# Optimization experiments

Measured on AMD Instinct MI355X. Metric: run time of the kernel, lower is better.

## Reference

```python
import jax, jax.numpy as jnp
import numpy as np

EPS = 1e-5

def _bn(h, gamma, beta):
    # BatchNorm1d in training mode: biased batch stats over the batch dim
    m = h.mean(axis=0)
    v = h.var(axis=0)
    return gamma * (h - m) * jax.lax.rsqrt(v + EPS) + beta


def setup_inputs() -> dict:
    key = jax.random.key(0)
    ks = jax.random.split(key, 8)
    N, E, D = 100000, 1000000, 64
    x = jax.random.normal(ks[0], (N, D), dtype=jnp.float32)
    pair_features = jax.random.normal(ks[1], (E, D), dtype=jnp.float32)
    pair_index = jax.random.randint(ks[2], (2, E), 0, N, dtype=jnp.int32)
    s = 1.0 / np.sqrt(D)
    W_atom = jax.random.uniform(ks[3], (D, D), jnp.float32, -s, s)
    b_atom = jnp.zeros((D,), jnp.float32)
    g_atom = jnp.ones((D,), jnp.float32)
    be_atom = jnp.zeros((D,), jnp.float32)
    W_pair = jax.random.uniform(ks[4], (D, D), jnp.float32, -s, s)
    b_pair = jnp.zeros((D,), jnp.float32)
    g_pair = jnp.ones((D,), jnp.float32)
    be_pair = jnp.zeros((D,), jnp.float32)
    s2 = 1.0 / np.sqrt(2 * D)
    W_a2p = jax.random.uniform(ks[5], (2 * D, D), jnp.float32, -s2, s2)
    b_a2p = jnp.zeros((D,), jnp.float32)
    return {
        "x": x, "pair_features": pair_features, "pair_index": pair_index,
        "W_atom": W_atom, "b_atom": b_atom, "g_atom": g_atom, "be_atom": be_atom,
        "W_pair": W_pair, "b_pair": b_pair, "g_pair": g_pair, "be_pair": be_pair,
        "W_a2p": W_a2p, "b_a2p": b_a2p,
    }


def reference(x, pair_features, pair_index,
              W_atom, b_atom, g_atom, be_atom,
              W_pair, b_pair, g_pair, be_pair,
              W_a2p, b_a2p):
    # atom path: Linear -> ReLU -> BatchNorm
    atom_out = _bn(jax.nn.relu(x @ W_atom + b_atom), g_atom, be_atom)
    # pair path: gather send/recv atoms, concat, linear
    send = x[pair_index[0]]                       # [E, D]
    recv = x[pair_index[1]]                       # [E, D]
    pair_input = jnp.concatenate([send, recv], axis=-1)  # [E, 2D]
    a2p = pair_input @ W_a2p + b_a2p              # [E, Dp]
    pair_bn = _bn(jax.nn.relu(pair_features @ W_pair + b_pair), g_pair, be_pair)
    return atom_out, a2p + pair_bn
```

## Files before the change

kernel.cpp:

```cpp
#include <hip/hip_runtime.h>

#define D 64
#define EPS 1e-5f

typedef __bf16 bf16x8 __attribute__((ext_vector_type(8)));
typedef float  f32x4  __attribute__((ext_vector_type(4)));

#define MFMA(a, b, c) __builtin_amdgcn_mfma_f32_16x16x32_bf16((a), (b), (c), 0, 0, 0)

static inline int imin(int a, int b) { return a < b ? a : b; }

template <bool NTLOAD>
__global__ void __launch_bounds__(256) fused_h_stats_kernel(
    const float* __restrict__ in, const float* __restrict__ W,
    const float* __restrict__ bias, int nrows,
    float* __restrict__ stats, __bf16* __restrict__ hout)
{
    const int tid = threadIdx.x;
    const int lane = tid & 63, wv = tid >> 6;
    const int q = lane >> 4, l16 = lane & 15;

    bf16x8 Bf[2][4];
#pragma unroll
    for (int ks = 0; ks < 2; ++ks)
#pragma unroll
      for (int nt = 0; nt < 4; ++nt)
#pragma unroll
        for (int j = 0; j < 8; ++j)
          Bf[ks][nt][j] = (__bf16)W[(ks * 32 + q * 8 + j) * 64 + nt * 16 + l16];

    float bc[4];
#pragma unroll
    for (int nt = 0; nt < 4; ++nt) bc[nt] = bias[nt * 16 + l16];

    float s[4] = {0.f, 0.f, 0.f, 0.f}, sq[4] = {0.f, 0.f, 0.f, 0.f};
    const f32x4 ZERO = {0.f, 0.f, 0.f, 0.f};

    const int ntiles = (nrows + 31) >> 5;
    const int stride = gridDim.x << 2;
    for (int t = (blockIdx.x << 2) + wv; t < ntiles; t += stride) {
        f32x4 st[2][2][2];
#pragma unroll
        for (int mt = 0; mt < 2; ++mt) {
            int arow = (t << 5) + mt * 16 + l16;
            arow = arow < nrows ? arow : nrows - 1;
            const float* p = in + (size_t)arow * 64 + q * 8;
#pragma unroll
            for (int ks = 0; ks < 2; ++ks) {
                if (NTLOAD) {
                    st[mt][ks][0] = __builtin_nontemporal_load((const f32x4*)(p + ks * 32));
                    st[mt][ks][1] = __builtin_nontemporal_load((const f32x4*)(p + ks * 32 + 4));
                } else {
                    st[mt][ks][0] = *(const f32x4*)(p + ks * 32);
                    st[mt][ks][1] = *(const f32x4*)(p + ks * 32 + 4);
                }
            }
        }

        bf16x8 af[2][2];
#pragma unroll
        for (int mt = 0; mt < 2; ++mt)
#pragma unroll
          for (int ks = 0; ks < 2; ++ks)
#pragma unroll
            for (int j = 0; j < 8; ++j)
              af[mt][ks][j] = (__bf16)st[mt][ks][j >> 2][j & 3];

        f32x4 acc[2][4];
#pragma unroll
        for (int mt = 0; mt < 2; ++mt)
#pragma unroll
          for (int nt = 0; nt < 4; ++nt) {
            acc[mt][nt] = MFMA(af[mt][0], Bf[0][nt], ZERO);
            acc[mt][nt] = MFMA(af[mt][1], Bf[1][nt], acc[mt][nt]);
          }

#pragma unroll
        for (int mt = 0; mt < 2; ++mt) {
            bf16x8 hh[2];
#pragma unroll
            for (int nt = 0; nt < 4; ++nt)
#pragma unroll
              for (int r = 0; r < 4; ++r) {
                const int row = (t << 5) + mt * 16 + q * 4 + r;
                float h = fmaxf(acc[mt][nt][r] + bc[nt], 0.f);
                if (row < nrows) { s[nt] += h; sq[nt] = fmaf(h, h, sq[nt]); }
                hh[nt >> 1][(nt & 1) * 4 + r] = (__bf16)h;
              }
            if (((2 * t + mt) << 4) < nrows) {
                __bf16* dst = hout + ((size_t)(2 * t + mt) * 2048 + lane * 16);
                *(bf16x8*)dst = hh[0];
                *(bf16x8*)(dst + 8) = hh[1];
            }
        }
    }

#pragma unroll
    for (int nt = 0; nt < 4; ++nt) {
        s[nt]  += __shfl_xor(s[nt], 16, 64);  s[nt]  += __shfl_xor(s[nt], 32, 64);
        sq[nt] += __shfl_xor(sq[nt], 16, 64); sq[nt] += __shfl_xor(sq[nt], 32, 64);
    }
    if (q == 0) {
#pragma unroll
        for (int nt = 0; nt < 4; ++nt) {
            atomicAdd(&stats[nt * 16 + l16], s[nt]);
            atomicAdd(&stats[64 + nt * 16 + l16], sq[nt]);
        }
    }
}

__global__ void finalize_stats_kernel(
    const float* __restrict__ stats,
    const float* __restrict__ g_a, const float* __restrict__ be_a,
    const float* __restrict__ g_p, const float* __restrict__ be_p,
    float n_atom, float n_pair, float* __restrict__ params)
{
    const int t = threadIdx.x;
    const int j = t & 63;
    const bool p = t >= 64;
    const float* st = stats + (p ? 128 : 0);
    const float* g  = p ? g_p  : g_a;
    const float* be = p ? be_p : be_a;
    const float cnt = p ? n_pair : n_atom;
    float m = st[j] / cnt;
    float v = st[64 + j] / cnt - m * m;
    float sc = g[j] * rsqrtf(v + EPS);
    float sh = be[j] - m * sc;
    float* pr = params + (p ? 128 : 0);
    pr[j] = sc;
    pr[64 + j] = sh;
}

__global__ void __launch_bounds__(256) apply_atom_kernel(
    float* __restrict__ out, const float* __restrict__ params, int nrows)
{
    const int tid = threadIdx.x;
    const int lane = tid & 63, wv = tid >> 6;
    const int q = lane >> 4, l16 = lane & 15;

    float sc[4], sh[4];
#pragma unroll
    for (int nt = 0; nt < 4; ++nt) {
        sc[nt] = params[nt * 16 + l16];
        sh[nt] = params[64 + nt * 16 + l16];
    }

    const int ntiles = (nrows + 15) >> 4;
    const int stride = gridDim.x << 2;
    for (int t = (blockIdx.x << 2) + wv; t < ntiles; t += stride) {
        const __bf16* src = (const __bf16*)out + ((size_t)t * 2048 + lane * 16);
        bf16x8 h0 = *(const bf16x8*)src;
        bf16x8 h1 = *(const bf16x8*)(src + 8);
        asm volatile("s_waitcnt vmcnt(0)" ::: "memory");
#pragma unroll
        for (int nt = 0; nt < 4; ++nt)
#pragma unroll
          for (int r = 0; r < 4; ++r) {
            const int row = (t << 4) + q * 4 + r;
            float h = (float)((nt < 2) ? h0[nt * 4 + r] : h1[(nt - 2) * 4 + r]);
            if (row < nrows)
                __builtin_nontemporal_store(fmaf(h, sc[nt], sh[nt]),
                                            out + (size_t)row * 64 + nt * 16 + l16);
          }
    }
}

__global__ void __launch_bounds__(256) pair_pass2_kernel(
    float* __restrict__ out, const float* __restrict__ x,
    const int* __restrict__ pidx,
    const float* __restrict__ Wa, const float* __restrict__ ba,
    int E, const float* __restrict__ params)
{
    const int tid = threadIdx.x;
    const int lane = tid & 63, wv = tid >> 6;
    const int q = lane >> 4, l16 = lane & 15;

    bf16x8 B2[4][4];
#pragma unroll
    for (int ks = 0; ks < 4; ++ks)
#pragma unroll
      for (int nt = 0; nt < 4; ++nt)
#pragma unroll
        for (int j = 0; j < 8; ++j)
          B2[ks][nt][j] = (__bf16)Wa[(ks * 32 + q * 8 + j) * 64 + nt * 16 + l16];

    float bac[4], sc[4], sh[4];
#pragma unroll
    for (int nt = 0; nt < 4; ++nt) {
        bac[nt] = ba[nt * 16 + l16];
        sc[nt]  = params[nt * 16 + l16];
        sh[nt]  = params[64 + nt * 16 + l16];
    }

    const f32x4 ZERO = {0.f, 0.f, 0.f, 0.f};

    const int ntiles = E >> 4;
    const int stride = gridDim.x << 2;
    for (int t = (blockIdx.x << 2) + wv; t < ntiles; t += stride) {
        const int e0 = t << 4;
        const int se = pidx[e0 + l16];
        const int re = pidx[E + e0 + l16];
        const float* ps = x + (size_t)se * 64 + q * 8;
        const float* pr = x + (size_t)re * 64 + q * 8;

        f32x4 g[4][2];
        g[0][0] = *(const f32x4*)ps;          g[0][1] = *(const f32x4*)(ps + 4);
        g[1][0] = *(const f32x4*)(ps + 32);   g[1][1] = *(const f32x4*)(ps + 36);
        g[2][0] = *(const f32x4*)pr;          g[2][1] = *(const f32x4*)(pr + 4);
        g[3][0] = *(const f32x4*)(pr + 32);   g[3][1] = *(const f32x4*)(pr + 36);

        const __bf16* hsrc = (const __bf16*)out + ((size_t)t * 2048 + lane * 16);
        bf16x8 h0 = *(const bf16x8*)hsrc;
        bf16x8 h1 = *(const bf16x8*)(hsrc + 8);

        bf16x8 af[4];
#pragma unroll
        for (int ks = 0; ks < 4; ++ks)
#pragma unroll
          for (int j = 0; j < 8; ++j)
            af[ks][j] = (__bf16)g[ks][j >> 2][j & 3];

        f32x4 acc[4];
#pragma unroll
        for (int nt = 0; nt < 4; ++nt) acc[nt] = ZERO;
#pragma unroll
        for (int ks = 0; ks < 4; ++ks)
#pragma unroll
          for (int nt = 0; nt < 4; ++nt)
            acc[nt] = MFMA(af[ks], B2[ks][nt], acc[nt]);

        asm volatile("s_waitcnt vmcnt(0)" ::: "memory");
#pragma unroll
        for (int nt = 0; nt < 4; ++nt)
#pragma unroll
          for (int r = 0; r < 4; ++r) {
            float h = (float)((nt < 2) ? h0[nt * 4 + r] : h1[(nt - 2) * 4 + r]);
            float val = fmaf(h, sc[nt], sh[nt]) + acc[nt][r] + bac[nt];
            __builtin_nontemporal_store(val,
                out + (size_t)(e0 + q * 4 + r) * 64 + nt * 16 + l16);
          }
    }
}

extern "C" void kernel_launch(void* const* d_in, const int* in_sizes, int n_in,
                              void* d_out, int out_size, void* d_ws, size_t ws_size,
                              hipStream_t stream) {
    const float* x       = (const float*)d_in[0];
    const float* pf      = (const float*)d_in[1];
    const int*   pidx    = (const int*)d_in[2];
    const float* W_atom  = (const float*)d_in[3];
    const float* b_atom  = (const float*)d_in[4];
    const float* g_atom  = (const float*)d_in[5];
    const float* be_atom = (const float*)d_in[6];
    const float* W_pair  = (const float*)d_in[7];
    const float* b_pair  = (const float*)d_in[8];
    const float* g_pair  = (const float*)d_in[9];
    const float* be_pair = (const float*)d_in[10];
    const float* W_a2p   = (const float*)d_in[11];
    const float* b_a2p   = (const float*)d_in[12];

    const int N = in_sizes[0] / D;
    const int E = in_sizes[1] / D;

    float* out_atom = (float*)d_out;
    float* out_pair = out_atom + (size_t)N * D;

    float* stats  = (float*)d_ws;
    float* params = stats + 256;

    (void)hipMemsetAsync(d_ws, 0, 256 * sizeof(float), stream);

    const int ta = (N + 31) / 32, tp = (E + 31) / 32;
    const int ga = imin((ta + 3) / 4, 2048);
    const int gp = imin((tp + 3) / 4, 2048);

    fused_h_stats_kernel<false><<<ga, 256, 0, stream>>>(
        x, W_atom, b_atom, N, stats, (__bf16*)out_atom);
    fused_h_stats_kernel<true><<<gp, 256, 0, stream>>>(
        pf, W_pair, b_pair, E, stats + 128, (__bf16*)out_pair);

    finalize_stats_kernel<<<1, 128, 0, stream>>>(stats, g_atom, be_atom,
                                                 g_pair, be_pair,
                                                 (float)N, (float)E, params);

    const int t16a = (N + 15) / 16, t16p = E / 16;
    apply_atom_kernel<<<imin((t16a + 3) / 4, 2048), 256, 0, stream>>>(
        out_atom, params, N);
    pair_pass2_kernel<<<imin((t16p + 3) / 4, 2048), 256, 0, stream>>>(
        out_pair, x, pidx, W_a2p, b_a2p, E, params + 128);
}
```

Before: 824.8 us.

## Coalesce tile loads via LDS transpose and prefetch next tile in h/stats kernel

The first-pass kernel now loads each 32-row tile with fully contiguous lane-strided float4 reads, converts to bf16, and stages it through a per-wave LDS buffer with padded stride before reading the MFMA A fragments. It also software-pipelines the loop by issuing the next tile's global loads before processing the current one, and halves the grid cap so each wave handles more tiles. The aim is better coalescing and latency hiding on the memory-bound pass over the 1M-row pair features. The cost is extra LDS traffic, more registers, and fewer resident blocks.

Measured after the change: 721.9 us. -12.5%, faster.

```diff
diff --git a/kernel.cpp b/kernel.cpp
--- a/kernel.cpp
+++ b/kernel.cpp
@@ -3,12 +3,15 @@
 #define D 64
 #define EPS 1e-5f
 
+typedef __bf16 bf16x4 __attribute__((ext_vector_type(4)));
 typedef __bf16 bf16x8 __attribute__((ext_vector_type(8)));
 typedef float  f32x4  __attribute__((ext_vector_type(4)));
 
 #define MFMA(a, b, c) __builtin_amdgcn_mfma_f32_16x16x32_bf16((a), (b), (c), 0, 0, 0)
 
 static inline int imin(int a, int b) { return a < b ? a : b; }
+
+#define LDS_STRIDE 80
 
 template <bool NTLOAD>
 __global__ void __launch_bounds__(256) fused_h_stats_kernel(
@@ -16,9 +19,11 @@
     const float* __restrict__ bias, int nrows,
     float* __restrict__ stats, __bf16* __restrict__ hout)
 {
+    __shared__ __bf16 lds[4][32 * LDS_STRIDE];
     const int tid = threadIdx.x;
     const int lane = tid & 63, wv = tid >> 6;
     const int q = lane >> 4, l16 = lane & 15;
+    __bf16* my = lds[wv];
 
     bf16x8 Bf[2][4];
 #pragma unroll
@@ -38,33 +43,55 @@
 
     const int ntiles = (nrows + 31) >> 5;
     const int stride = gridDim.x << 2;
-    for (int t = (blockIdx.x << 2) + wv; t < ntiles; t += stride) {
-        f32x4 st[2][2][2];
-#pragma unroll
-        for (int mt = 0; mt < 2; ++mt) {
-            int arow = (t << 5) + mt * 16 + l16;
-            arow = arow < nrows ? arow : nrows - 1;
-            const float* p = in + (size_t)arow * 64 + q * 8;
-#pragma unroll
-            for (int ks = 0; ks < 2; ++ks) {
-                if (NTLOAD) {
-                    st[mt][ks][0] = __builtin_nontemporal_load((const f32x4*)(p + ks * 32));
-                    st[mt][ks][1] = __builtin_nontemporal_load((const f32x4*)(p + ks * 32 + 4));
-                } else {
-                    st[mt][ks][0] = *(const f32x4*)(p + ks * 32);
-                    st[mt][ks][1] = *(const f32x4*)(p + ks * 32 + 4);
-                }
+
+    auto LOADTILE = [&](int tt, f32x4* ld) {
+        const int row0 = tt << 5;
+        if (row0 + 32 <= nrows) {
+            const float* tb = in + (size_t)row0 * 64 + lane * 4;
+#pragma unroll
+            for (int i = 0; i < 8; ++i)
+                ld[i] = NTLOAD ? __builtin_nontemporal_load((const f32x4*)(tb + i * 256))
+                               : *(const f32x4*)(tb + i * 256);
+        } else {
+#pragma unroll
+            for (int i = 0; i < 8; ++i) {
+                int row = row0 + i * 4 + (lane >> 4);
+                ld[i] = (row < nrows)
+                          ? *(const f32x4*)(in + (size_t)row * 64 + (lane & 15) * 4)
+                          : ZERO;
             }
         }
+    };
+
+    int t = (blockIdx.x << 2) + wv;
+    bool valid = t < ntiles;
+    f32x4 ld[8];
+    if (valid) LOADTILE(t, ld);
+
+    while (valid) {
+        bf16x4 c[8];
+#pragma unroll
+        for (int i = 0; i < 8; ++i)
+#pragma unroll
+          for (int j = 0; j < 4; ++j)
+            c[i][j] = (__bf16)ld[i][j];
+
+        const int tn = t + stride;
+        const bool vn = tn < ntiles;
+        if (vn) LOADTILE(tn, ld);
+
+#pragma unroll
+        for (int i = 0; i < 8; ++i) {
+            int wrow = i * 4 + (lane >> 4);
+            *(bf16x4*)&my[wrow * LDS_STRIDE + (lane & 15) * 4] = c[i];
+        }
 
         bf16x8 af[2][2];
 #pragma unroll
         for (int mt = 0; mt < 2; ++mt)
 #pragma unroll
           for (int ks = 0; ks < 2; ++ks)
-#pragma unroll
-            for (int j = 0; j < 8; ++j)
-              af[mt][ks][j] = (__bf16)st[mt][ks][j >> 2][j & 3];
+            af[mt][ks] = *(const bf16x8*)&my[(mt * 16 + l16) * LDS_STRIDE + ks * 32 + q * 8];
 
         f32x4 acc[2][4];
 #pragma unroll
@@ -93,6 +120,8 @@
                 *(bf16x8*)(dst + 8) = hh[1];
             }
         }
+
+        t = tn; valid = vn;
     }
 
 #pragma unroll
@@ -271,8 +300,8 @@
     (void)hipMemsetAsync(d_ws, 0, 256 * sizeof(float), stream);
 
     const int ta = (N + 31) / 32, tp = (E + 31) / 32;
-    const int ga = imin((ta + 3) / 4, 2048);
-    const int gp = imin((tp + 3) / 4, 2048);
+    const int ga = imin((ta + 3) / 4, 1024);
+    const int gp = imin((tp + 3) / 4, 1024);
 
     fused_h_stats_kernel<false><<<ga, 256, 0, stream>>>(
         x, W_atom, b_atom, N, stats, (__bf16*)out_atom);
```
